# Kernel optimization log

Hardware: AMD Instinct MI355X
Metric: run time of the kernel (lower is better)

The kernel has to match this reference:

```python
import jax, jax.numpy as jnp
import numpy as np

NUM_FREQ = 32
MAX_POS = 10000.0
COORD_DIM = 3
EMB_DIM = COORD_DIM * NUM_FREQ * 2  # 192
KIN = 2 * EMB_DIM                   # 384
C = 32
T = 4
N_Y = 50000
N_X = 32768
K = 8
E = N_X * K
MLP_DIMS = [KIN, 128, 256, 128, C]


def sinusoidal_embed(p):
    # transformer-style sinusoidal embedding: [n, d] -> [n, d*NUM_FREQ*2]
    freqs = (1.0 / MAX_POS) ** (jnp.arange(NUM_FREQ, dtype=p.dtype) / NUM_FREQ)
    ang = p[..., None] * freqs                       # [n, d, nf]
    emb = jnp.stack([jnp.sin(ang), jnp.cos(ang)], axis=-1)  # [n, d, nf, 2]
    return emb.reshape(p.shape[0], -1)


def setup_inputs() -> dict:
    key = jax.random.key(0)
    ks = jax.random.split(key, 16)
    inp = {
        "y": jax.random.uniform(ks[0], (N_Y, COORD_DIM), dtype=jnp.float32),
        "x": jax.random.uniform(ks[1], (N_X, COORD_DIM), dtype=jnp.float32),
        "f_y": jax.random.normal(ks[2], (T, N_Y, C), dtype=jnp.float32),
        "neighbors_index": jax.random.randint(ks[3], (E,), 0, N_Y, dtype=jnp.int64),
    }
    # channel MLP params: 384 -> 128 -> 256 -> 128 -> 32, gelu between layers
    for i in range(4):
        fan_in, fan_out = MLP_DIMS[i], MLP_DIMS[i + 1]
        s = 1.0 / np.sqrt(fan_in)
        inp[f"W{i}"] = jax.random.uniform(ks[4 + 2 * i], (fan_in, fan_out), jnp.float32, -s, s)
        inp[f"b{i}"] = jax.random.uniform(ks[5 + 2 * i], (fan_out,), jnp.float32, -s, s)
    return inp


def reference(y, x, f_y, neighbors_index, W0, b0, W1, b1, W2, b2, W3, b3):
    n_x = x.shape[0]
    k = neighbors_index.shape[0] // n_x
    y_emb = sinusoidal_embed(y)            # [n_y, 192]
    x_emb = sinusoidal_embed(x)            # [n_x, 192]
    rep = y_emb[neighbors_index]           # [E, 192] gather per edge
    slf = jnp.repeat(x_emb, k, axis=0)     # [E, 192] query embedding per edge
    h = jnp.concatenate([rep, slf], axis=-1)  # [E, 384]
    h = jax.nn.gelu(h @ W0 + b0)
    h = jax.nn.gelu(h @ W1 + b1)
    h = jax.nn.gelu(h @ W2 + b2)
    kern = h @ W3 + b3                     # [E, C] kernel values
    in_feat = f_y[:, neighbors_index, :]   # [T, E, C] gathered source features
    prod = kern[None, :, :] * in_feat      # linear transform: k(x,y) * f(y)
    # reduction='sum' over each query's neighborhood (uniform K segments)
    out = prod.reshape(f_y.shape[0], n_x, k, -1).sum(axis=2)  # [T, n_x, C]
    return out
```

## Files before the change

### kernel.cpp

```cpp
#include <hip/hip_runtime.h>
#include <stdint.h>

#define EMB_DIM 192
#define CDIM 32
#define TDIM 4
#define N_Y 50000
#define N_X 32768
#define KNBR 8
#define ECNT (N_X*KNBR)
#define NTILE 4096
#define NBLK 768

#define H1S 134
#define H2S 262
#define KS  33
#define ES  200

typedef __attribute__((ext_vector_type(8))) short bf16x8;
typedef __attribute__((ext_vector_type(4))) float f32x4;

static __device__ __forceinline__ short f2bf(float f){
  unsigned u = __float_as_uint(f);
  return (short)((u + 0x7FFFu) >> 16);
}
static __device__ __forceinline__ unsigned pk_bf16(float lo, float hi){
#if defined(__has_builtin)
#if __has_builtin(__builtin_amdgcn_cvt_pk_bf16_f32)
  typedef __attribute__((ext_vector_type(2))) __bf16 bf16x2_t;
  bf16x2_t v = __builtin_amdgcn_cvt_pk_bf16_f32(lo, hi);
  return *(unsigned*)&v;
#else
  return ((__float_as_uint(lo) + 0x7FFFu) >> 16) |
         ((((__float_as_uint(hi) + 0x7FFFu) >> 16)) << 16);
#endif
#else
  return ((__float_as_uint(lo) + 0x7FFFu) >> 16) |
         ((((__float_as_uint(hi) + 0x7FFFu) >> 16)) << 16);
#endif
}
static __device__ __forceinline__ float geluf(float x){
  float x2 = x * x;
  float u  = __builtin_fmaf(0.044715f, x2, 1.0f);
  float p  = x * -1.5957691216057308f;
  float e  = __expf(p * u);
  return x * __builtin_amdgcn_rcpf(1.0f + e);
}
static __device__ __forceinline__ void barrier_lds(){
  asm volatile("s_waitcnt lgkmcnt(0)\n\ts_barrier" ::: "memory");
}

__global__ __launch_bounds__(256) void transpose_all(
    const float* __restrict__ W0, const float* __restrict__ W1,
    const float* __restrict__ W2, const float* __restrict__ W3,
    short* __restrict__ w0yt, short* __restrict__ w0xt,
    short* __restrict__ w1t, short* __restrict__ w2t, short* __restrict__ w3t){
  int id = blockIdx.x * 256 + threadIdx.x;
  if (id < 24576) {
    int n = id / 192, k = id - n * 192;
    w0yt[id] = f2bf(W0[k * 128 + n]);
  } else if (id < 49152) {
    int loc = id - 24576; int n = loc / 192, k = loc - n * 192;
    w0xt[loc] = f2bf(W0[(k + 192) * 128 + n]);
  } else if (id < 81920) {
    int loc = id - 49152; int n = loc / 128, k = loc - n * 128;
    w1t[loc] = f2bf(W1[k * 256 + n]);
  } else if (id < 114688) {
    int loc = id - 81920; int n = loc / 256, k = loc - n * 256;
    w2t[loc] = f2bf(W2[k * 128 + n]);
  } else if (id < 118784) {
    int loc = id - 114688; int n = loc / 128, k = loc - n * 128;
    w3t[loc] = f2bf(W3[k * 32 + n]);
  }
}

__global__ __launch_bounds__(256, 2) void precompute_c(
    const float* __restrict__ ypts, const float* __restrict__ xpts,
    const short* __restrict__ w0yt, const short* __restrict__ w0xt,
    const float* __restrict__ b0,
    short* __restrict__ c_y, float* __restrict__ c_x)
{
  __shared__ __attribute__((aligned(16))) short s_e[64 * ES];
  const int tid = threadIdx.x;
  const bool isY = blockIdx.x < 782;
  const int row0 = isY ? blockIdx.x * 64 : (blockIdx.x - 782) * 64;
  const int wave = tid >> 6, lane = tid & 63;
  const int quad = lane >> 4, l15 = lane & 15;

  {
    const int r = tid >> 2, q = tid & 3;
    const int grow = row0 + r;
    const bool valid = isY ? (grow < N_Y) : true;
    const float* src = isY ? (ypts + (size_t)grow * 3) : (xpts + (size_t)grow * 3);
    float c[3] = {0.f, 0.f, 0.f};
    if (valid) { c[0] = src[0]; c[1] = src[1]; c[2] = src[2]; }
    #pragma unroll
    for (int j = 0; j < 24; ++j) {
      int p = q * 24 + j;
      int d = p >> 5, i = p & 31;
      float f = __expf(-0.28782313662425575f * (float)i);
      float s, co;
      __sincosf(c[d] * f, &s, &co);
      *(unsigned*)&s_e[r * ES + d * 64 + 2 * i] = pk_bf16(s, co);
    }
  }
  __syncthreads();

  const short* w0t = isY ? w0yt : w0xt;
  f32x4 acc[4][2];
  #pragma unroll
  for (int mt = 0; mt < 4; ++mt)
    #pragma unroll
    for (int nt = 0; nt < 2; ++nt) acc[mt][nt] = (f32x4){0.f, 0.f, 0.f, 0.f};
  #pragma unroll
  for (int ch = 0; ch < 6; ++ch) {
    bf16x8 a[4], b[2];
    #pragma unroll
    for (int mt = 0; mt < 4; ++mt)
      a[mt] = *(const bf16x8*)&s_e[(mt * 16 + l15) * ES + ch * 32 + quad * 8];
    #pragma unroll
    for (int nt = 0; nt < 2; ++nt)
      b[nt] = *(const bf16x8*)&w0t[(size_t)(wave * 32 + nt * 16 + l15) * 192 + ch * 32 + quad * 8];
    #pragma unroll
    for (int mt = 0; mt < 4; ++mt)
      #pragma unroll
      for (int nt = 0; nt < 2; ++nt)
        acc[mt][nt] = __builtin_amdgcn_mfma_f32_16x16x32_bf16(a[mt], b[nt], acc[mt][nt], 0, 0, 0);
  }
  #pragma unroll
  for (int nt = 0; nt < 2; ++nt) {
    int col = wave * 32 + nt * 16 + l15;
    float bias = isY ? 0.f : b0[col];
    #pragma unroll
    for (int mt = 0; mt < 4; ++mt)
      #pragma unroll
      for (int rg = 0; rg < 4; ++rg) {
        int grow = row0 + mt * 16 + quad * 4 + rg;
        if (isY) { if (grow < N_Y) c_y[(size_t)grow * 128 + col] = f2bf(acc[mt][nt][rg]); }
        else     { c_x[(size_t)grow * 128 + col] = acc[mt][nt][rg] + bias; }
      }
  }
}

__global__ __launch_bounds__(256, 3) void fused_edge(
    const short* __restrict__ c_y, const float* __restrict__ c_x,
    const int* __restrict__ nidx, const float* __restrict__ f_y,
    const short* __restrict__ w1t, const float* __restrict__ b1,
    const short* __restrict__ w2t, const float* __restrict__ b2,
    const short* __restrict__ w3t, const float* __restrict__ b3,
    float* __restrict__ out)
{
  __shared__ __attribute__((aligned(16))) char smem[50688];
  short* s_h2   = (short*)smem;
  float* s_kern = (float*)smem;
  short* s_h1   = (short*)(smem + 33536);

  const int tid  = threadIdx.x;
  const int wave = tid >> 6, lane = tid & 63;
  const int quad = lane >> 4, l15 = lane & 15;
  const int r    = tid >> 2, q = tid & 3;
  const int xloc = tid >> 5, cc = tid & 31;

  int   pf_idx1;
  uint4 pf_cy[4];
  {
    int idx0 = nidx[blockIdx.x * 64 + r];
    const uint4* cyp = (const uint4*)(c_y + (size_t)idx0 * 128 + q * 32);
    #pragma unroll
    for (int i = 0; i < 4; ++i) pf_cy[i] = cyp[i];
    int t1 = blockIdx.x + NBLK; if (t1 >= NTILE) t1 = blockIdx.x;
    pf_idx1 = nidx[t1 * 64 + r];
  }

  for (int tile = blockIdx.x; tile < NTILE; tile += NBLK) {
    const int e0 = tile * 64;

    {
      float4 cxv[8];
      const float4* cxp = (const float4*)(c_x + (size_t)((e0 + r) >> 3) * 128 + q * 32);
      #pragma unroll
      for (int i = 0; i < 8; ++i) cxv[i] = cxp[i];
      const float* cxa = (const float*)cxv;
      const unsigned* cya = (const unsigned*)pf_cy;
      unsigned pk[16];
      #pragma unroll
      for (int jj = 0; jj < 16; ++jj) {
        unsigned u = cya[jj];
        float lo = __uint_as_float(u << 16)         + cxa[2 * jj];
        float hi = __uint_as_float(u & 0xffff0000u) + cxa[2 * jj + 1];
        pk[jj] = pk_bf16(geluf(lo), geluf(hi));
      }
      uint4* dst = (uint4*)&s_h1[r * H1S + q * 32];
      #pragma unroll
      for (int jj = 0; jj < 4; ++jj)
        dst[jj] = *(uint4*)&pk[jj * 4];
    }

    {
      const uint4* cyp = (const uint4*)(c_y + (size_t)pf_idx1 * 128 + q * 32);
      #pragma unroll
      for (int i = 0; i < 4; ++i) pf_cy[i] = cyp[i];
      int t2 = tile + 2 * NBLK; if (t2 >= NTILE) t2 = tile;
      pf_idx1 = nidx[t2 * 64 + r];
    }

    barrier_lds();

    {
      f32x4 acc1[4][4];
      #pragma unroll
      for (int mt = 0; mt < 4; ++mt)
        #pragma unroll
        for (int nt = 0; nt < 4; ++nt) acc1[mt][nt] = (f32x4){0.f, 0.f, 0.f, 0.f};
      #pragma unroll
      for (int ch = 0; ch < 4; ++ch) {
        bf16x8 a[4], b[4];
        #pragma unroll
        for (int mt = 0; mt < 4; ++mt)
          a[mt] = *(const bf16x8*)&s_h1[(mt * 16 + l15) * H1S + ch * 32 + quad * 8];
        #pragma unroll
        for (int nt = 0; nt < 4; ++nt)
          b[nt] = *(const bf16x8*)&w1t[(size_t)(wave * 64 + nt * 16 + l15) * 128 + ch * 32 + quad * 8];
        #pragma unroll
        for (int mt = 0; mt < 4; ++mt)
          #pragma unroll
          for (int nt = 0; nt < 4; ++nt)
            acc1[mt][nt] = __builtin_amdgcn_mfma_f32_16x16x32_bf16(a[mt], b[nt], acc1[mt][nt], 0, 0, 0);
      }
      #pragma unroll
      for (int nt = 0; nt < 4; ++nt) {
        int col = wave * 64 + nt * 16 + l15;
        float bias = b1[col];
        #pragma unroll
        for (int mt = 0; mt < 4; ++mt)
          #pragma unroll
          for (int rg = 0; rg < 4; ++rg) {
            int row = mt * 16 + quad * 4 + rg;
            s_h2[row * H2S + col] = f2bf(geluf(acc1[mt][nt][rg] + bias));
          }
      }
    }
    barrier_lds();

    float fv[32];
    {
      f32x4 acc2[4][2];
      #pragma unroll
      for (int mt = 0; mt < 4; ++mt)
        #pragma unroll
        for (int nt = 0; nt < 2; ++nt) acc2[mt][nt] = (f32x4){0.f, 0.f, 0.f, 0.f};
      #pragma unroll
      for (int ch = 0; ch < 8; ++ch) {
        bf16x8 a[4], b[2];
        #pragma unroll
        for (int mt = 0; mt < 4; ++mt)
          a[mt] = *(const bf16x8*)&s_h2[(mt * 16 + l15) * H2S + ch * 32 + quad * 8];
        #pragma unroll
        for (int nt = 0; nt < 2; ++nt)
          b[nt] = *(const bf16x8*)&w2t[(size_t)(wave * 32 + nt * 16 + l15) * 256 + ch * 32 + quad * 8];
        #pragma unroll
        for (int mt = 0; mt < 4; ++mt)
          #pragma unroll
          for (int nt = 0; nt < 2; ++nt)
            acc2[mt][nt] = __builtin_amdgcn_mfma_f32_16x16x32_bf16(a[mt], b[nt], acc2[mt][nt], 0, 0, 0);
      }

      #pragma unroll
      for (int j = 0; j < KNBR; ++j) {
        int idx = nidx[e0 + xloc * 8 + j];
        const float* fp = f_y + (size_t)idx * CDIM + cc;
        #pragma unroll
        for (int t = 0; t < TDIM; ++t)
          fv[j * 4 + t] = fp[(size_t)t * N_Y * CDIM];
      }

      #pragma unroll
      for (int nt = 0; nt < 2; ++nt) {
        int col = wave * 32 + nt * 16 + l15;
        float bias = b2[col];
        #pragma unroll
        for (int mt = 0; mt < 4; ++mt)
          #pragma unroll
          for (int rg = 0; rg < 4; ++rg) {
            int row = mt * 16 + quad * 4 + rg;
            s_h1[row * H1S + col] = f2bf(geluf(acc2[mt][nt][rg] + bias));
          }
      }
    }
    barrier_lds();

    {
      f32x4 acc3[2];
      acc3[0] = (f32x4){0.f, 0.f, 0.f, 0.f};
      acc3[1] = (f32x4){0.f, 0.f, 0.f, 0.f};
      #pragma unroll
      for (int ch = 0; ch < 4; ++ch) {
        bf16x8 a3 = *(const bf16x8*)&s_h1[(wave * 16 + l15) * H1S + ch * 32 + quad * 8];
        #pragma unroll
        for (int nt = 0; nt < 2; ++nt) {
          bf16x8 b3f = *(const bf16x8*)&w3t[(size_t)(nt * 16 + l15) * 128 + ch * 32 + quad * 8];
          acc3[nt] = __builtin_amdgcn_mfma_f32_16x16x32_bf16(a3, b3f, acc3[nt], 0, 0, 0);
        }
      }
      #pragma unroll
      for (int nt = 0; nt < 2; ++nt) {
        int col = nt * 16 + l15;
        float bias = b3[col];
        #pragma unroll
        for (int rg = 0; rg < 4; ++rg) {
          int row = wave * 16 + quad * 4 + rg;
          s_kern[row * KS + col] = acc3[nt][rg] + bias;
        }
      }
    }
    barrier_lds();

    {
      float acc[TDIM] = {0.f, 0.f, 0.f, 0.f};
      const int ebase = xloc * 8;
      #pragma unroll
      for (int j = 0; j < KNBR; ++j) {
        float kv = s_kern[(ebase + j) * KS + cc];
        #pragma unroll
        for (int t = 0; t < TDIM; ++t)
          acc[t] += kv * fv[j * 4 + t];
      }
      const int xg = tile * 8 + xloc;
      #pragma unroll
      for (int t = 0; t < TDIM; ++t)
        out[((size_t)t * N_X + xg) * CDIM + cc] = acc[t];
    }
  }
}

extern "C" void kernel_launch(void* const* d_in, const int* in_sizes, int n_in,
                              void* d_out, int out_size, void* d_ws, size_t ws_size,
                              hipStream_t stream)
{
  const float* y   = (const float*)d_in[0];
  const float* x   = (const float*)d_in[1];
  const float* f_y = (const float*)d_in[2];
  const int*  nidx = (const int*)d_in[3];
  const float* W0 = (const float*)d_in[4];  const float* b0 = (const float*)d_in[5];
  const float* W1 = (const float*)d_in[6];  const float* b1 = (const float*)d_in[7];
  const float* W2 = (const float*)d_in[8];  const float* b2 = (const float*)d_in[9];
  const float* W3 = (const float*)d_in[10]; const float* b3 = (const float*)d_in[11];

  char* ws = (char*)d_ws;
  short* c_y  = (short*)(ws + 0);
  float* c_x  = (float*)(ws + 12800000);
  short* w0yt = (short*)(ws + 29577216);
  short* w0xt = (short*)(ws + 29626368);
  short* w1t  = (short*)(ws + 29675520);
  short* w2t  = (short*)(ws + 29741056);
  short* w3t  = (short*)(ws + 29806592);

  hipLaunchKernelGGL(transpose_all, dim3((118784 + 255) / 256), dim3(256), 0, stream,
                     W0, W1, W2, W3, w0yt, w0xt, w1t, w2t, w3t);
  hipLaunchKernelGGL(precompute_c, dim3(782 + 512), dim3(256), 0, stream,
                     y, x, w0yt, w0xt, b0, c_y, c_x);
  hipLaunchKernelGGL(fused_edge, dim3(NBLK), dim3(256), 0, stream,
                     c_y, c_x, nidx, f_y, w1t, b1, w2t, b2, w3t, b3, (float*)d_out);
}
```

Measured before the change: 276.2 us.

## Merge weight transpose into precompute kernel and defer f_y gather to reduction

Folds the W1/W2/W3 transpose into the precompute kernel as extra blocks, so one launch is removed. Each precompute block now loads W0 straight from fp32 global memory into registers as bf16, replacing the separate transposed W0 buffers. The f_y gather moves from before the layer-2 epilogue into the final reduction loop, which frees 32 registers but no longer overlaps those loads with MFMA work. It also drops the hardware packed bf16 convert in favour of the manual rounding path.

Result: slower. 313.6 us (+13.5%).

```diff
diff --git a/kernel.cpp b/kernel.cpp
--- a/kernel.cpp
+++ b/kernel.cpp
@@ -16,6 +16,11 @@
 #define KS  33
 #define ES  200
 
+#define PREP_TW 272
+#define PREP_Y0 PREP_TW
+#define PREP_X0 (PREP_TW + 782)
+#define PREP_NB (PREP_TW + 782 + 512)
+
 typedef __attribute__((ext_vector_type(8))) short bf16x8;
 typedef __attribute__((ext_vector_type(4))) float f32x4;
 
@@ -24,19 +29,8 @@
   return (short)((u + 0x7FFFu) >> 16);
 }
 static __device__ __forceinline__ unsigned pk_bf16(float lo, float hi){
-#if defined(__has_builtin)
-#if __has_builtin(__builtin_amdgcn_cvt_pk_bf16_f32)
-  typedef __attribute__((ext_vector_type(2))) __bf16 bf16x2_t;
-  bf16x2_t v = __builtin_amdgcn_cvt_pk_bf16_f32(lo, hi);
-  return *(unsigned*)&v;
-#else
   return ((__float_as_uint(lo) + 0x7FFFu) >> 16) |
          ((((__float_as_uint(hi) + 0x7FFFu) >> 16)) << 16);
-#endif
-#else
-  return ((__float_as_uint(lo) + 0x7FFFu) >> 16) |
-         ((((__float_as_uint(hi) + 0x7FFFu) >> 16)) << 16);
-#endif
 }
 static __device__ __forceinline__ float geluf(float x){
   float x2 = x * x;
@@ -49,42 +43,47 @@
   asm volatile("s_waitcnt lgkmcnt(0)\n\ts_barrier" ::: "memory");
 }
 
-__global__ __launch_bounds__(256) void transpose_all(
-    const float* __restrict__ W0, const float* __restrict__ W1,
-    const float* __restrict__ W2, const float* __restrict__ W3,
-    short* __restrict__ w0yt, short* __restrict__ w0xt,
-    short* __restrict__ w1t, short* __restrict__ w2t, short* __restrict__ w3t){
-  int id = blockIdx.x * 256 + threadIdx.x;
-  if (id < 24576) {
-    int n = id / 192, k = id - n * 192;
-    w0yt[id] = f2bf(W0[k * 128 + n]);
-  } else if (id < 49152) {
-    int loc = id - 24576; int n = loc / 192, k = loc - n * 192;
-    w0xt[loc] = f2bf(W0[(k + 192) * 128 + n]);
-  } else if (id < 81920) {
-    int loc = id - 49152; int n = loc / 128, k = loc - n * 128;
-    w1t[loc] = f2bf(W1[k * 256 + n]);
-  } else if (id < 114688) {
-    int loc = id - 81920; int n = loc / 256, k = loc - n * 256;
-    w2t[loc] = f2bf(W2[k * 128 + n]);
-  } else if (id < 118784) {
-    int loc = id - 114688; int n = loc / 128, k = loc - n * 128;
-    w3t[loc] = f2bf(W3[k * 32 + n]);
-  }
-}
-
-__global__ __launch_bounds__(256, 2) void precompute_c(
+__global__ __launch_bounds__(256, 2) void prep_all(
     const float* __restrict__ ypts, const float* __restrict__ xpts,
-    const short* __restrict__ w0yt, const short* __restrict__ w0xt,
-    const float* __restrict__ b0,
+    const float* __restrict__ W0, const float* __restrict__ b0,
+    const float* __restrict__ W1, const float* __restrict__ W2,
+    const float* __restrict__ W3,
+    short* __restrict__ w1t, short* __restrict__ w2t, short* __restrict__ w3t,
     short* __restrict__ c_y, float* __restrict__ c_x)
 {
+  const int tid = threadIdx.x;
+  if (blockIdx.x < PREP_TW) {
+    int id = blockIdx.x * 256 + tid;
+    if (id < 32768) {
+      int n = id >> 7, k = id & 127;
+      w1t[id] = f2bf(W1[k * 256 + n]);
+    } else if (id < 65536) {
+      int loc = id - 32768; int n = loc >> 8, k = loc & 255;
+      w2t[loc] = f2bf(W2[k * 128 + n]);
+    } else if (id < 69632) {
+      int loc = id - 65536; int n = loc >> 7, k = loc & 127;
+      w3t[loc] = f2bf(W3[k * 32 + n]);
+    }
+    return;
+  }
+
   __shared__ __attribute__((aligned(16))) short s_e[64 * ES];
-  const int tid = threadIdx.x;
-  const bool isY = blockIdx.x < 782;
-  const int row0 = isY ? blockIdx.x * 64 : (blockIdx.x - 782) * 64;
+  const bool isY = blockIdx.x < PREP_X0;
+  const int row0 = isY ? (blockIdx.x - PREP_Y0) * 64 : (blockIdx.x - PREP_X0) * 64;
   const int wave = tid >> 6, lane = tid & 63;
   const int quad = lane >> 4, l15 = lane & 15;
+  const float* W0h = W0 + (isY ? 0 : 192 * 128);
+
+  short bv[2][48];
+  #pragma unroll
+  for (int nt = 0; nt < 2; ++nt) {
+    int n = wave * 32 + nt * 16 + l15;
+    #pragma unroll
+    for (int ch = 0; ch < 6; ++ch)
+      #pragma unroll
+      for (int j = 0; j < 8; ++j)
+        bv[nt][ch * 8 + j] = f2bf(W0h[(size_t)(ch * 32 + quad * 8 + j) * 128 + n]);
+  }
 
   {
     const int r = tid >> 2, q = tid & 3;
@@ -105,7 +104,6 @@
   }
   __syncthreads();
 
-  const short* w0t = isY ? w0yt : w0xt;
   f32x4 acc[4][2];
   #pragma unroll
   for (int mt = 0; mt < 4; ++mt)
@@ -113,18 +111,16 @@
     for (int nt = 0; nt < 2; ++nt) acc[mt][nt] = (f32x4){0.f, 0.f, 0.f, 0.f};
   #pragma unroll
   for (int ch = 0; ch < 6; ++ch) {
-    bf16x8 a[4], b[2];
+    bf16x8 a[4];
     #pragma unroll
     for (int mt = 0; mt < 4; ++mt)
       a[mt] = *(const bf16x8*)&s_e[(mt * 16 + l15) * ES + ch * 32 + quad * 8];
     #pragma unroll
-    for (int nt = 0; nt < 2; ++nt)
-      b[nt] = *(const bf16x8*)&w0t[(size_t)(wave * 32 + nt * 16 + l15) * 192 + ch * 32 + quad * 8];
-    #pragma unroll
     for (int mt = 0; mt < 4; ++mt)
       #pragma unroll
       for (int nt = 0; nt < 2; ++nt)
-        acc[mt][nt] = __builtin_amdgcn_mfma_f32_16x16x32_bf16(a[mt], b[nt], acc[mt][nt], 0, 0, 0);
+        acc[mt][nt] = __builtin_amdgcn_mfma_f32_16x16x32_bf16(
+            a[mt], *(const bf16x8*)&bv[nt][ch * 8], acc[mt][nt], 0, 0, 0);
   }
   #pragma unroll
   for (int nt = 0; nt < 2; ++nt) {
@@ -194,7 +190,6 @@
       for (int jj = 0; jj < 4; ++jj)
         dst[jj] = *(uint4*)&pk[jj * 4];
     }
-
     {
       const uint4* cyp = (const uint4*)(c_y + (size_t)pf_idx1 * 128 + q * 32);
       #pragma unroll
@@ -202,7 +197,6 @@
       int t2 = tile + 2 * NBLK; if (t2 >= NTILE) t2 = tile;
       pf_idx1 = nidx[t2 * 64 + r];
     }
-
     barrier_lds();
 
     {
@@ -241,7 +235,6 @@
     }
     barrier_lds();
 
-    float fv[32];
     {
       f32x4 acc2[4][2];
       #pragma unroll
@@ -263,16 +256,6 @@
           for (int nt = 0; nt < 2; ++nt)
             acc2[mt][nt] = __builtin_amdgcn_mfma_f32_16x16x32_bf16(a[mt], b[nt], acc2[mt][nt], 0, 0, 0);
       }
-
-      #pragma unroll
-      for (int j = 0; j < KNBR; ++j) {
-        int idx = nidx[e0 + xloc * 8 + j];
-        const float* fp = f_y + (size_t)idx * CDIM + cc;
-        #pragma unroll
-        for (int t = 0; t < TDIM; ++t)
-          fv[j * 4 + t] = fp[(size_t)t * N_Y * CDIM];
-      }
-
       #pragma unroll
       for (int nt = 0; nt < 2; ++nt) {
         int col = wave * 32 + nt * 16 + l15;
@@ -320,9 +303,11 @@
       #pragma unroll
       for (int j = 0; j < KNBR; ++j) {
         float kv = s_kern[(ebase + j) * KS + cc];
+        int idx = nidx[e0 + ebase + j];
+        const float* fp = f_y + (size_t)idx * CDIM + cc;
         #pragma unroll
         for (int t = 0; t < TDIM; ++t)
-          acc[t] += kv * fv[j * 4 + t];
+          acc[t] += kv * fp[(size_t)t * N_Y * CDIM];
       }
       const int xg = tile * 8 + xloc;
       #pragma unroll
@@ -348,16 +333,12 @@
   char* ws = (char*)d_ws;
   short* c_y  = (short*)(ws + 0);
   float* c_x  = (float*)(ws + 12800000);
-  short* w0yt = (short*)(ws + 29577216);
-  short* w0xt = (short*)(ws + 29626368);
-  short* w1t  = (short*)(ws + 29675520);
-  short* w2t  = (short*)(ws + 29741056);
-  short* w3t  = (short*)(ws + 29806592);
-
-  hipLaunchKernelGGL(transpose_all, dim3((118784 + 255) / 256), dim3(256), 0, stream,
-                     W0, W1, W2, W3, w0yt, w0xt, w1t, w2t, w3t);
-  hipLaunchKernelGGL(precompute_c, dim3(782 + 512), dim3(256), 0, stream,
-                     y, x, w0yt, w0xt, b0, c_y, c_x);
+  short* w1t  = (short*)(ws + 29577216);
+  short* w2t  = (short*)(ws + 29642752);
+  short* w3t  = (short*)(ws + 29708288);
+
+  hipLaunchKernelGGL(prep_all, dim3(PREP_NB), dim3(256), 0, stream,
+                     y, x, W0, b0, W1, W2, W3, w1t, w2t, w3t, c_y, c_x);
   hipLaunchKernelGGL(fused_edge, dim3(NBLK), dim3(256), 0, stream,
                      c_y, c_x, nidx, f_y, w1t, b1, w2t, b2, w3t, b3, (float*)d_out);
 }
```
